# Kernel optimization log

Hardware: AMD Instinct MI355X
Metric: run time of the kernel (lower is better)

The kernel has to match this reference:

```python
import jax, jax.numpy as jnp
import numpy as np

B = 8; C = 128; EXP = 4; H = 112; W = 112; K = 3; PAD = 1; STRIDE = 1
IN_C = C * EXP  # 512
EPS = 1e-5


def setup_inputs() -> dict:
    key = jax.random.key(0)
    ks = jax.random.split(key, 24)
    f32 = jnp.float32

    def n(k, shape, s=0.05):
        return jax.random.normal(k, shape, f32) * s

    def bn_params(k):
        k1, k2, k3, k4 = jax.random.split(k, 4)
        g = 1.0 + 0.1 * jax.random.normal(k1, (), f32)  # placeholder, per-channel below
        return k1, k2, k3, k4

    inp = {}
    inp["x"] = jax.random.normal(ks[0], (B, IN_C, H, W), f32)
    # conv1: 1x1, 512 -> 128
    inp["w1"] = n(ks[1], (C, IN_C))
    inp["b1"] = n(ks[2], (C,))
    # bn1
    inp["g1"] = 1.0 + 0.1 * jax.random.normal(ks[3], (C,), f32)
    inp["be1"] = 0.1 * jax.random.normal(ks[4], (C,), f32)
    inp["m1"] = 0.1 * jax.random.normal(ks[5], (C,), f32)
    inp["v1"] = 1.0 + 0.1 * jax.random.uniform(ks[6], (C,), f32)
    # offset conv: 3x3, C -> 18 (small weights so sampling offsets stay modest)
    inp["woff"] = n(ks[7], (2 * K * K, C, K, K), 0.01)
    inp["boff"] = jnp.zeros((2 * K * K,), f32)
    # deformable conv weight: 3x3, C -> C
    inp["wd"] = n(ks[8], (C, C, K, K))
    inp["bd"] = n(ks[9], (C,))
    # bn2
    inp["g2"] = 1.0 + 0.1 * jax.random.normal(ks[10], (C,), f32)
    inp["be2"] = 0.1 * jax.random.normal(ks[11], (C,), f32)
    inp["m2"] = 0.1 * jax.random.normal(ks[12], (C,), f32)
    inp["v2"] = 1.0 + 0.1 * jax.random.uniform(ks[13], (C,), f32)
    # conv2: 1x1, 128 -> 512
    inp["w2"] = n(ks[14], (IN_C, C))
    inp["b2"] = n(ks[15], (IN_C,))
    # bn3
    inp["g3"] = 1.0 + 0.1 * jax.random.normal(ks[16], (IN_C,), f32)
    inp["be3"] = 0.1 * jax.random.normal(ks[17], (IN_C,), f32)
    inp["m3"] = 0.1 * jax.random.normal(ks[18], (IN_C,), f32)
    inp["v3"] = 1.0 + 0.1 * jax.random.uniform(ks[19], (IN_C,), f32)
    return inp


def conv1x1(x, w, b):
    return jnp.einsum("oc,bchw->bohw", w, x) + b[None, :, None, None]


def bn(x, g, be, m, v):
    inv = g / jnp.sqrt(v + EPS)
    return x * inv[None, :, None, None] + (be - m * inv)[None, :, None, None]


def conv3x3(x, w, b):
    out = jax.lax.conv_general_dilated(
        x, w, (STRIDE, STRIDE), ((PAD, PAD), (PAD, PAD)),
        dimension_numbers=("NCHW", "OIHW", "NCHW"))
    return out + b[None, :, None, None]


def deform_conv(x, offset, w, b):
    # x: [B, Cin, H, W]; offset: [B, 2*K*K, Ho, Wo] (y,x interleaved per kernel pt)
    Bn, Cin, Hh, Ww = x.shape
    Ho, Wo = offset.shape[2], offset.shape[3]
    P = Ho * Wo
    off = offset.reshape(Bn, K * K, 2, Ho, Wo)
    kk = jnp.arange(K * K)
    ky = (kk // K).astype(jnp.float32)  # 0..2
    kx = (kk % K).astype(jnp.float32)
    base_y = jnp.arange(Ho, dtype=jnp.float32) * STRIDE - PAD
    base_x = jnp.arange(Wo, dtype=jnp.float32) * STRIDE - PAD
    py = base_y[None, None, :, None] + ky[None, :, None, None] + off[:, :, 0]  # [B,9,Ho,Wo]
    px = base_x[None, None, None, :] + kx[None, :, None, None] + off[:, :, 1]
    y0 = jnp.floor(py); x0 = jnp.floor(px)
    dy = (py - y0).reshape(Bn, 1, -1)  # [B,1,9*P]
    dx = (px - x0).reshape(Bn, 1, -1)
    x_flat = x.reshape(Bn, Cin, Hh * Ww)

    def gather(yi, xi):
        valid = ((yi >= 0) & (yi <= Hh - 1) & (xi >= 0) & (xi <= Ww - 1))
        yc = jnp.clip(yi, 0, Hh - 1).astype(jnp.int32)
        xc = jnp.clip(xi, 0, Ww - 1).astype(jnp.int32)
        idx = (yc * Ww + xc).reshape(Bn, -1)  # [B, 9*P]
        g = jax.vmap(lambda xb, ib: xb[:, ib])(x_flat, idx)  # [B, Cin, 9*P]
        return g * valid.reshape(Bn, 1, -1).astype(x.dtype)

    v00 = gather(y0, x0)
    v01 = gather(y0, x0 + 1)
    v10 = gather(y0 + 1, x0)
    v11 = gather(y0 + 1, x0 + 1)
    cols = (v00 * (1 - dy) * (1 - dx) + v01 * (1 - dy) * dx
            + v10 * dy * (1 - dx) + v11 * dy * dx)  # [B, Cin, 9*P]
    cols = cols.reshape(Bn, Cin * K * K, P)
    out = jnp.einsum("oi,bip->bop", w.reshape(w.shape[0], -1), cols)
    out = out + b[None, :, None]
    return out.reshape(Bn, w.shape[0], Ho, Wo)


def reference(x, w1, b1, g1, be1, m1, v1, woff, boff, wd, bd,
              g2, be2, m2, v2, w2, b2, g3, be3, m3, v3):
    out = jax.nn.relu(bn(conv1x1(x, w1, b1), g1, be1, m1, v1))
    offset = conv3x3(out, woff, boff)
    out = deform_conv(out, offset, wd, bd)
    out = bn(out, g2, be2, m2, v2)
    out = bn(conv1x1(out, w2, b2), g3, be3, m3, v3)
    return jax.nn.relu(out + x)
```

## Files before the change

kernel.cpp:

```cpp
#include <hip/hip_runtime.h>
#include <hip/hip_bf16.h>


typedef __attribute__((ext_vector_type(8))) short short8;
typedef __attribute__((ext_vector_type(4))) float f32x4;

constexpr int Bn = 8;
constexpr int IC = 512;
constexpr int Cc = 128;
constexpr int Hh = 112;
constexpr int Ww = 112;
constexpr int Pp = Hh * Ww;
constexpr float EPSf = 1e-5f;

constexpr size_t OFS_OFFS  = 0;
constexpr size_t OFS_OUT2B = 2097152;
constexpr size_t OFS_W1B   = (size_t)Bn * Pp * IC / 2;
constexpr size_t OFS_W2B   = OFS_W1B + (size_t)Cc * IC / 2;
constexpr size_t OFS_WDB   = OFS_W2B + (size_t)IC * Cc / 2;
constexpr size_t OFS_WOFB  = OFS_WDB + (size_t)9 * Cc * Cc / 2;

__device__ __forceinline__ ushort f2bf(float f) {
  uint u = __float_as_uint(f);
  return (ushort)((u + 0x7fffu + ((u >> 16) & 1u)) >> 16);
}
__device__ __forceinline__ float bfLO(uint u) {
  return __uint_as_float(u << 16);
}
__device__ __forceinline__ float bfHI(uint u) {
  return __uint_as_float(u & 0xffff0000u);
}
__device__ __forceinline__ uint cvtpk(float a, float b) {
  __hip_bfloat162 h = __float22bfloat162_rn(make_float2(a, b));
  return *(uint*)&h;
}

__global__ __launch_bounds__(256) void prep_kernel(
    const float* __restrict__ w1, const float* __restrict__ w2,
    const float* __restrict__ wd, const float* __restrict__ woff,
    float* __restrict__ ws) {
  ushort* w1b  = (ushort*)(ws + OFS_W1B);
  ushort* w2b  = (ushort*)(ws + OFS_W2B);
  ushort* wdb  = (ushort*)(ws + OFS_WDB);
  ushort* wofb = (ushort*)(ws + OFS_WOFB);
  const int n1 = Cc * IC;
  const int n2 = IC * Cc;
  const int n3 = 9 * Cc * Cc;
  const int n4 = 9 * 32 * Cc;
  const int total = n1 + n2 + n3 + n4;
  for (int idx = blockIdx.x * blockDim.x + threadIdx.x; idx < total;
       idx += gridDim.x * blockDim.x) {
    if (idx < n1) {
      w1b[idx] = f2bf(w1[idx]);
    } else if (idx < n1 + n2) {
      int t = idx - n1;
      w2b[t] = f2bf(w2[t]);
    } else if (idx < n1 + n2 + n3) {
      int t = idx - n1 - n2;
      int k = t / (Cc * Cc), r = t % (Cc * Cc);
      int oc = r / Cc, ic = r % Cc;
      wdb[t] = f2bf(wd[(oc * Cc + ic) * 9 + k]);
    } else {
      int t = idx - n1 - n2 - n3;
      int k = t / (32 * Cc), r = t % (32 * Cc);
      int oc = r / Cc, ic = r % Cc;
      wofb[t] = (oc < 18) ? f2bf(woff[(oc * Cc + ic) * 9 + k]) : (ushort)0;
    }
  }
}

__global__ __launch_bounds__(256) void k1_fused_mfma(
    const float* __restrict__ x, const ushort* __restrict__ w1b,
    const float* __restrict__ b1, const float* __restrict__ g1,
    const float* __restrict__ be1, const float* __restrict__ m1,
    const float* __restrict__ v1, ushort* __restrict__ out1b) {
  __shared__ ushort At[64][136];

  const int tid = threadIdx.x;
  const int lane = tid & 63;
  const int wv = tid >> 6;
  const int lr = lane & 15, lg = lane >> 4;
  const int orig = blockIdx.x;
  const int bid = (orig & 7) * 196 + (orig >> 3);
  const int bi = bid / 196;
  const int p0 = (bid % 196) * 64;

  const int ic2 = (tid >> 2) * 2;
  const int pq = (tid & 3) * 4;

  const ushort* Bw = w1b + (size_t)(wv * 32) * IC;
  const float* xbase = x + (size_t)bi * IC * Pp + p0 + pq;

  f32x4 acc[4][2];
#pragma unroll
  for (int m = 0; m < 4; ++m) { acc[m][0] = (f32x4)0.f; acc[m][1] = (f32x4)0.f; }

  float4 pv0[4], pv1[4];
  {
    const float* r0 = xbase + (size_t)ic2 * Pp;
    const float* r1 = r0 + Pp;
#pragma unroll
    for (int i = 0; i < 4; ++i) {
      pv0[i] = *(const float4*)(r0 + 16 * i);
      pv1[i] = *(const float4*)(r1 + 16 * i);
    }
  }

#pragma unroll
  for (int ch = 0; ch < 4; ++ch) {
    const int c0 = ch * 128;
#pragma unroll
    for (int i = 0; i < 4; ++i) {
      int px = pq + 16 * i;
      *(uint*)&At[px + 0][ic2] = cvtpk(pv0[i].x, pv1[i].x);
      *(uint*)&At[px + 1][ic2] = cvtpk(pv0[i].y, pv1[i].y);
      *(uint*)&At[px + 2][ic2] = cvtpk(pv0[i].z, pv1[i].z);
      *(uint*)&At[px + 3][ic2] = cvtpk(pv0[i].w, pv1[i].w);
    }
    __syncthreads();

    if (ch < 3) {
      const float* r0 = xbase + (size_t)(c0 + 128 + ic2) * Pp;
      const float* r1 = r0 + Pp;
#pragma unroll
      for (int i = 0; i < 4; ++i) {
        pv0[i] = *(const float4*)(r0 + 16 * i);
        pv1[i] = *(const float4*)(r1 + 16 * i);
      }
    }

#pragma unroll
    for (int ks = 0; ks < 4; ++ks) {
      short8 b0 = *(const short8*)(Bw + (size_t)lr * IC + c0 + ks * 32 + 8 * lg);
      short8 b1v = *(const short8*)(Bw + (size_t)(16 + lr) * IC + c0 + ks * 32 + 8 * lg);
#pragma unroll
      for (int m = 0; m < 4; ++m) {
        short8 a = *(const short8*)&At[m * 16 + lr][ks * 32 + 8 * lg];
        acc[m][0] = __builtin_amdgcn_mfma_f32_16x16x32_bf16(a, b0, acc[m][0], 0, 0, 0);
        acc[m][1] = __builtin_amdgcn_mfma_f32_16x16x32_bf16(a, b1v, acc[m][1], 0, 0, 0);
      }
    }
    __syncthreads();
  }

#pragma unroll
  for (int n = 0; n < 2; ++n) {
    int oc = wv * 32 + n * 16 + lr;
    float inv = g1[oc] * rsqrtf(v1[oc] + EPSf);
    float sh = (b1[oc] - m1[oc]) * inv + be1[oc];
#pragma unroll
    for (int m = 0; m < 4; ++m) {
#pragma unroll
      for (int r = 0; r < 4; ++r) {
        int p = p0 + m * 16 + lg * 4 + r;
        out1b[((size_t)bi * Pp + p) * Cc + oc] =
            f2bf(fmaxf(acc[m][n][r] * inv + sh, 0.f));
      }
    }
  }
}

__global__ __launch_bounds__(256) void k2_offset_mfma(
    const ushort* __restrict__ out1b, const ushort* __restrict__ wofb,
    const float* __restrict__ boff, float* __restrict__ offs) {
  const int tid = threadIdx.x;
  const int lane = tid & 63;
  const int wv = tid >> 6;
  const int lr = lane & 15, lg = lane >> 4;
  const int orig = blockIdx.x;
  const int bid = (orig & 7) * 49 + (orig >> 3);
  const int bi = bid / 49;
  const int p0 = (bid % 49) * 256 + wv * 64;

  const ushort* src = out1b + (size_t)bi * Pp * Cc;

  int ohm[4], owm[4];
#pragma unroll
  for (int m = 0; m < 4; ++m) {
    int p = p0 + m * 16 + lr;
    ohm[m] = p / Ww;
    owm[m] = p - ohm[m] * Ww;
  }

  f32x4 acc[4][2];
#pragma unroll
  for (int m = 0; m < 4; ++m) { acc[m][0] = (f32x4)0.f; acc[m][1] = (f32x4)0.f; }

  for (int k = 0; k < 9; ++k) {
    const int kdy = k / 3 - 1, kdx = k % 3 - 1;
    const ushort* rp[4];
    bool val[4];
#pragma unroll
    for (int m = 0; m < 4; ++m) {
      int yy = ohm[m] + kdy, xx = owm[m] + kdx;
      val[m] = ((unsigned)yy < (unsigned)Hh) && ((unsigned)xx < (unsigned)Ww);
      int yc = min(max(yy, 0), Hh - 1), xc = min(max(xx, 0), Ww - 1);
      rp[m] = src + (size_t)(yc * Ww + xc) * Cc;
    }
#pragma unroll
    for (int ks = 0; ks < 4; ++ks) {
      short8 b0 = *(const short8*)(wofb + (size_t)(k * 32 + lr) * Cc + ks * 32 + 8 * lg);
      short8 b1v = *(const short8*)(wofb + (size_t)(k * 32 + 16 + lr) * Cc + ks * 32 + 8 * lg);
#pragma unroll
      for (int m = 0; m < 4; ++m) {
        short8 av = *(const short8*)(rp[m] + ks * 32 + 8 * lg);
        short8 a = val[m] ? av : (short8)0;
        acc[m][0] = __builtin_amdgcn_mfma_f32_16x16x32_bf16(a, b0, acc[m][0], 0, 0, 0);
        acc[m][1] = __builtin_amdgcn_mfma_f32_16x16x32_bf16(a, b1v, acc[m][1], 0, 0, 0);
      }
    }
  }

#pragma unroll
  for (int n = 0; n < 2; ++n) {
    int oc = n * 16 + lr;
    if (oc < 18) {
      float bo = boff[oc];
      float* orow = offs + ((size_t)bi * 18 + oc) * Pp;
#pragma unroll
      for (int m = 0; m < 4; ++m) {
        int p = p0 + m * 16 + lg * 4;
        float4 o;
        o.x = acc[m][n][0] + bo;
        o.y = acc[m][n][1] + bo;
        o.z = acc[m][n][2] + bo;
        o.w = acc[m][n][3] + bo;
        *(float4*)(orow + p) = o;
      }
    }
  }
}

__global__ __launch_bounds__(256) void k3_deform_mfma(
    const ushort* __restrict__ out1b, const float* __restrict__ offs,
    const ushort* __restrict__ wdb, const float* __restrict__ bd,
    const float* __restrict__ g2, const float* __restrict__ be2,
    const float* __restrict__ m2, const float* __restrict__ v2,
    ushort* __restrict__ out2b) {
  __shared__ ushort colsA[64][136];
  __shared__ float meta[9 * 64 * 8];

  const int tid = threadIdx.x;
  const int lane = tid & 63;
  const int wv = tid >> 6;
  const int lr = lane & 15, lg = lane >> 4;
  const int orig = blockIdx.x;
  const int bid = (orig & 7) * 196 + (orig >> 3);
  const int bi = bid / 196;
  const int p0 = (bid % 196) * 64;

  const ushort* src = out1b + (size_t)bi * Pp * Cc;
  const float* offb = offs + (size_t)bi * 18 * Pp;

  {
    const int p = p0 + lane;
    const int oh = p / Ww, ow = p - oh * Ww;
    for (int k = wv; k < 9; k += 4) {
      const int kdy = k / 3 - 1, kdx = k % 3 - 1;
      float py = (float)(oh + kdy) + offb[(size_t)(2 * k) * Pp + p];
      float pxf = (float)(ow + kdx) + offb[(size_t)(2 * k + 1) * Pp + p];
      float y0f = floorf(py), x0f = floorf(pxf);
      float dy = py - y0f, dx = pxf - x0f;
      int y0 = (int)y0f, x0 = (int)x0f;
      int y1 = y0 + 1, x1 = x0 + 1;
      float wy0 = (y0 >= 0 && y0 < Hh) ? 1.f - dy : 0.f;
      float wy1 = (y1 >= 0 && y1 < Hh) ? dy : 0.f;
      float wx0 = (x0 >= 0 && x0 < Ww) ? 1.f - dx : 0.f;
      float wx1 = (x1 >= 0 && x1 < Ww) ? dx : 0.f;
      int yc0 = min(max(y0, 0), Hh - 1), yc1 = min(max(y1, 0), Hh - 1);
      int xc0 = min(max(x0, 0), Ww - 1), xc1 = min(max(x1, 0), Ww - 1);
      float* mp = &meta[(k * 64 + lane) * 8];
      mp[0] = wy0 * wx0;
      mp[1] = wy0 * wx1;
      mp[2] = wy1 * wx0;
      mp[3] = wy1 * wx1;
      int* ip = (int*)(mp + 4);
      ip[0] = (yc0 * Ww + xc0) * (Cc * 2);
      ip[1] = (yc0 * Ww + xc1) * (Cc * 2);
      ip[2] = (yc1 * Ww + xc0) * (Cc * 2);
      ip[3] = (yc1 * Ww + xc1) * (Cc * 2);
    }
  }
  __syncthreads();

  f32x4 acc[4][2];
#pragma unroll
  for (int m = 0; m < 4; ++m) { acc[m][0] = (f32x4)0.f; acc[m][1] = (f32x4)0.f; }

  const int half = lane >> 5;
  const int l32 = lane & 31;
  const char* sb = (const char*)src + l32 * 8;

  for (int k = 0; k < 9; ++k) {
#pragma unroll 4
    for (int t = 0; t < 8; ++t) {
      const int px = wv * 16 + 2 * t + half;
      const float* mp = &meta[(k * 64 + px) * 8];
      float4 w4 = *(const float4*)mp;
      int4 o4 = *(const int4*)(mp + 4);
      uint2 v00 = *(const uint2*)(sb + o4.x);
      uint2 v01 = *(const uint2*)(sb + o4.y);
      uint2 v10 = *(const uint2*)(sb + o4.z);
      uint2 v11 = *(const uint2*)(sb + o4.w);
      float c0 = w4.x * bfLO(v00.x) + w4.y * bfLO(v01.x)
               + w4.z * bfLO(v10.x) + w4.w * bfLO(v11.x);
      float c1 = w4.x * bfHI(v00.x) + w4.y * bfHI(v01.x)
               + w4.z * bfHI(v10.x) + w4.w * bfHI(v11.x);
      float c2 = w4.x * bfLO(v00.y) + w4.y * bfLO(v01.y)
               + w4.z * bfLO(v10.y) + w4.w * bfLO(v11.y);
      float c3 = w4.x * bfHI(v00.y) + w4.y * bfHI(v01.y)
               + w4.z * bfHI(v10.y) + w4.w * bfHI(v11.y);
      uint2 packed;
      packed.x = cvtpk(c0, c1);
      packed.y = cvtpk(c2, c3);
      *(uint2*)&colsA[px][l32 * 4] = packed;
    }
    __syncthreads();

    const ushort* wk = wdb + (size_t)k * Cc * Cc + (size_t)(wv * 32) * Cc;
#pragma unroll
    for (int ks = 0; ks < 4; ++ks) {
      short8 b0 = *(const short8*)(wk + lr * Cc + ks * 32 + 8 * lg);
      short8 b1v = *(const short8*)(wk + (16 + lr) * Cc + ks * 32 + 8 * lg);
#pragma unroll
      for (int m = 0; m < 4; ++m) {
        short8 a = *(const short8*)&colsA[m * 16 + lr][ks * 32 + 8 * lg];
        acc[m][0] = __builtin_amdgcn_mfma_f32_16x16x32_bf16(a, b0, acc[m][0], 0, 0, 0);
        acc[m][1] = __builtin_amdgcn_mfma_f32_16x16x32_bf16(a, b1v, acc[m][1], 0, 0, 0);
      }
    }
    __syncthreads();
  }

#pragma unroll
  for (int n = 0; n < 2; ++n) {
    int oc = wv * 32 + n * 16 + lr;
    float inv = g2[oc] * rsqrtf(v2[oc] + EPSf);
    float sh = (bd[oc] - m2[oc]) * inv + be2[oc];
#pragma unroll
    for (int m = 0; m < 4; ++m) {
#pragma unroll
      for (int r = 0; r < 4; ++r) {
        int p = p0 + m * 16 + lg * 4 + r;
        out2b[((size_t)bi * Pp + p) * Cc + oc] = f2bf(acc[m][n][r] * inv + sh);
      }
    }
  }
}

__global__ __launch_bounds__(256, 2) void k4_mfma(
    const ushort* __restrict__ out2b, const ushort* __restrict__ w2b,
    const float* __restrict__ b2, const float* __restrict__ g3,
    const float* __restrict__ be3, const float* __restrict__ m3,
    const float* __restrict__ v3, const float* __restrict__ x,
    float* __restrict__ out) {
  const int tid = threadIdx.x;
  const int lane = tid & 63;
  const int wv = tid >> 6;
  const int lr = lane & 15, lg = lane >> 4;
  const int orig = blockIdx.x;
  const int bid = (orig & 7) * 392 + (orig >> 3);
  const int bi = bid / 392;
  const int r392 = bid % 392;
  const int oc_t = r392 / 49;
  const int p0 = (r392 % 49) * 256 + wv * 64;
  const int ocb = oc_t * 64;

  const ushort* A = out2b + ((size_t)bi * Pp + p0) * Cc;
  const ushort* Bw = w2b + (size_t)ocb * Cc;

  float4 xv[4][4];
#pragma unroll
  for (int n = 0; n < 4; ++n) {
    int oc = ocb + n * 16 + lr;
    const float* xr = x + ((size_t)bi * IC + oc) * Pp + p0 + lg * 4;
#pragma unroll
    for (int m = 0; m < 4; ++m) xv[n][m] = *(const float4*)(xr + m * 16);
  }

  f32x4 acc[4][4];
#pragma unroll
  for (int m = 0; m < 4; ++m)
#pragma unroll
    for (int n = 0; n < 4; ++n) acc[m][n] = (f32x4)0.f;

#pragma unroll
  for (int ks = 0; ks < 4; ++ks) {
    short8 a[4];
#pragma unroll
    for (int m = 0; m < 4; ++m)
      a[m] = *(const short8*)(A + (size_t)(m * 16 + lr) * Cc + ks * 32 + 8 * lg);
#pragma unroll
    for (int n = 0; n < 4; ++n) {
      short8 b = *(const short8*)(Bw + (size_t)(n * 16 + lr) * Cc + ks * 32 + 8 * lg);
#pragma unroll
      for (int m = 0; m < 4; ++m)
        acc[m][n] = __builtin_amdgcn_mfma_f32_16x16x32_bf16(a[m], b, acc[m][n], 0, 0, 0);
    }
  }

#pragma unroll
  for (int n = 0; n < 4; ++n) {
    int oc = ocb + n * 16 + lr;
    float inv = g3[oc] * rsqrtf(v3[oc] + EPSf);
    float sh = (b2[oc] - m3[oc]) * inv + be3[oc];
    float* orow = out + ((size_t)bi * IC + oc) * Pp + p0 + lg * 4;
#pragma unroll
    for (int m = 0; m < 4; ++m) {
      float4 o;
      o.x = fmaxf(acc[m][n][0] * inv + sh + xv[n][m].x, 0.f);
      o.y = fmaxf(acc[m][n][1] * inv + sh + xv[n][m].y, 0.f);
      o.z = fmaxf(acc[m][n][2] * inv + sh + xv[n][m].z, 0.f);
      o.w = fmaxf(acc[m][n][3] * inv + sh + xv[n][m].w, 0.f);
      *(float4*)(orow + m * 16) = o;
    }
  }
}

extern "C" void kernel_launch(void* const* d_in, const int* in_sizes, int n_in,
                              void* d_out, int out_size, void* d_ws, size_t ws_size,
                              hipStream_t stream) {
  const float* x    = (const float*)d_in[0];
  const float* w1   = (const float*)d_in[1];
  const float* b1   = (const float*)d_in[2];
  const float* g1   = (const float*)d_in[3];
  const float* be1  = (const float*)d_in[4];
  const float* m1   = (const float*)d_in[5];
  const float* v1   = (const float*)d_in[6];
  const float* woff = (const float*)d_in[7];
  const float* boff = (const float*)d_in[8];
  const float* wd   = (const float*)d_in[9];
  const float* bd   = (const float*)d_in[10];
  const float* g2   = (const float*)d_in[11];
  const float* be2  = (const float*)d_in[12];
  const float* m2   = (const float*)d_in[13];
  const float* v2   = (const float*)d_in[14];
  const float* w2   = (const float*)d_in[15];
  const float* b2   = (const float*)d_in[16];
  const float* g3   = (const float*)d_in[17];
  const float* be3  = (const float*)d_in[18];
  const float* m3   = (const float*)d_in[19];
  const float* v3   = (const float*)d_in[20];

  float* ws   = (float*)d_ws;
  float* out  = (float*)d_out;
  float*  offs  = ws + OFS_OFFS;
  ushort* out2b = (ushort*)(ws + OFS_OUT2B);
  ushort* w1b   = (ushort*)(ws + OFS_W1B);
  ushort* w2b   = (ushort*)(ws + OFS_W2B);
  ushort* wdb   = (ushort*)(ws + OFS_WDB);
  ushort* wofb  = (ushort*)(ws + OFS_WOFB);
  ushort* out1b = (ushort*)d_out;

  prep_kernel<<<512, 256, 0, stream>>>(w1, w2, wd, woff, ws);
  k1_fused_mfma<<<Bn * 196, 256, 0, stream>>>(x, w1b, b1, g1, be1, m1, v1, out1b);
  k2_offset_mfma<<<Bn * 49, 256, 0, stream>>>(out1b, wofb, boff, offs);
  k3_deform_mfma<<<Bn * 196, 256, 0, stream>>>(out1b, offs, wdb, bd,
                                               g2, be2, m2, v2, out2b);
  k4_mfma<<<Bn * 392, 256, 0, stream>>>(out2b, w2b, b2, g3, be3, m3, v3, x, out);
}
```

Before: 373.6 us.

## Double-buffer deformable column tile and overlap bilinear gathers with MFMA

The deform kernel now keeps two column buffers in LDS. Gathers for the next kernel tap are issued before the current tap's MFMA work and committed in halves between its k-steps, so gather latency is hidden behind matrix math. Each lane also gathers 16-byte vectors covering 8 channels, where it used to take 8 bytes, so a quarter-wave handles one pixel. This adds LDS usage and holds many more gathered values in registers, which could lower occupancy. It also removes one barrier per tap.

```diff
diff --git a/kernel.cpp b/kernel.cpp
--- a/kernel.cpp
+++ b/kernel.cpp
@@ -237,7 +237,7 @@
     const float* __restrict__ g2, const float* __restrict__ be2,
     const float* __restrict__ m2, const float* __restrict__ v2,
     ushort* __restrict__ out2b) {
-  __shared__ ushort colsA[64][136];
+  __shared__ ushort colsA[2][64][136];
   __shared__ float meta[9 * 64 * 8];
 
   const int tid = threadIdx.x;
@@ -287,50 +287,89 @@
 #pragma unroll
   for (int m = 0; m < 4; ++m) { acc[m][0] = (f32x4)0.f; acc[m][1] = (f32x4)0.f; }
 
-  const int half = lane >> 5;
-  const int l32 = lane & 31;
-  const char* sb = (const char*)src + l32 * 8;
+  const int pxq = lane >> 4;
+  const int l16 = lane & 15;
+  const char* sb = (const char*)src + l16 * 16;
+
+  uint4 gv[4][4];
+  float4 gw[4];
+
+#define ISSUE(kk, t)                                                     \
+  {                                                                      \
+    const int px_ = wv * 16 + (t) * 4 + pxq;                             \
+    const float* mp_ = &meta[((kk) * 64 + px_) * 8];                     \
+    gw[t] = *(const float4*)mp_;                                         \
+    int4 o4_ = *(const int4*)(mp_ + 4);                                  \
+    gv[t][0] = *(const uint4*)(sb + o4_.x);                              \
+    gv[t][1] = *(const uint4*)(sb + o4_.y);                              \
+    gv[t][2] = *(const uint4*)(sb + o4_.z);                              \
+    gv[t][3] = *(const uint4*)(sb + o4_.w);                              \
+  }
+
+#define COMMIT(buf, t)                                                   \
+  {                                                                      \
+    const int px_ = wv * 16 + (t) * 4 + pxq;                             \
+    float4 w4_ = gw[t];                                                  \
+    uint4 pk_;                                                           \
+    uint* pkp_ = (uint*)&pk_;                                            \
+    _Pragma("unroll")                                                    \
+    for (int j = 0; j < 4; ++j) {                                        \
+      uint a0_ = ((const uint*)&gv[t][0])[j];                            \
+      uint a1_ = ((const uint*)&gv[t][1])[j];                            \
+      uint a2_ = ((const uint*)&gv[t][2])[j];                            \
+      uint a3_ = ((const uint*)&gv[t][3])[j];                            \
+      float lo_ = w4_.x * bfLO(a0_) + w4_.y * bfLO(a1_)                  \
+                + w4_.z * bfLO(a2_) + w4_.w * bfLO(a3_);                 \
+      float hi_ = w4_.x * bfHI(a0_) + w4_.y * bfHI(a1_)                  \
+                + w4_.z * bfHI(a2_) + w4_.w * bfHI(a3_);                 \
+      pkp_[j] = cvtpk(lo_, hi_);                                         \
+    }                                                                    \
+    *(uint4*)&colsA[buf][px_][l16 * 8] = pk_;                            \
+  }
+
+  ISSUE(0, 0) ISSUE(0, 1) ISSUE(0, 2) ISSUE(0, 3)
+  COMMIT(0, 0) COMMIT(0, 1) COMMIT(0, 2) COMMIT(0, 3)
+  __syncthreads();
 
   for (int k = 0; k < 9; ++k) {
-#pragma unroll 4
-    for (int t = 0; t < 8; ++t) {
-      const int px = wv * 16 + 2 * t + half;
-      const float* mp = &meta[(k * 64 + px) * 8];
-      float4 w4 = *(const float4*)mp;
-      int4 o4 = *(const int4*)(mp + 4);
-      uint2 v00 = *(const uint2*)(sb + o4.x);
-      uint2 v01 = *(const uint2*)(sb + o4.y);
-      uint2 v10 = *(const uint2*)(sb + o4.z);
-      uint2 v11 = *(const uint2*)(sb + o4.w);
-      float c0 = w4.x * bfLO(v00.x) + w4.y * bfLO(v01.x)
-               + w4.z * bfLO(v10.x) + w4.w * bfLO(v11.x);
-      float c1 = w4.x * bfHI(v00.x) + w4.y * bfHI(v01.x)
-               + w4.z * bfHI(v10.x) + w4.w * bfHI(v11.x);
-      float c2 = w4.x * bfLO(v00.y) + w4.y * bfLO(v01.y)
-               + w4.z * bfLO(v10.y) + w4.w * bfLO(v11.y);
-      float c3 = w4.x * bfHI(v00.y) + w4.y * bfHI(v01.y)
-               + w4.z * bfHI(v10.y) + w4.w * bfHI(v11.y);
-      uint2 packed;
-      packed.x = cvtpk(c0, c1);
-      packed.y = cvtpk(c2, c3);
-      *(uint2*)&colsA[px][l32 * 4] = packed;
-    }
-    __syncthreads();
-
+    const int cur = k & 1;
+    const int nxt = cur ^ 1;
     const ushort* wk = wdb + (size_t)k * Cc * Cc + (size_t)(wv * 32) * Cc;
-#pragma unroll
-    for (int ks = 0; ks < 4; ++ks) {
+
+    if (k < 8) { ISSUE(k + 1, 0) ISSUE(k + 1, 1) }
+
+#pragma unroll
+    for (int ks = 0; ks < 2; ++ks) {
       short8 b0 = *(const short8*)(wk + lr * Cc + ks * 32 + 8 * lg);
       short8 b1v = *(const short8*)(wk + (16 + lr) * Cc + ks * 32 + 8 * lg);
 #pragma unroll
       for (int m = 0; m < 4; ++m) {
-        short8 a = *(const short8*)&colsA[m * 16 + lr][ks * 32 + 8 * lg];
+        short8 a = *(const short8*)&colsA[cur][m * 16 + lr][ks * 32 + 8 * lg];
         acc[m][0] = __builtin_amdgcn_mfma_f32_16x16x32_bf16(a, b0, acc[m][0], 0, 0, 0);
         acc[m][1] = __builtin_amdgcn_mfma_f32_16x16x32_bf16(a, b1v, acc[m][1], 0, 0, 0);
       }
     }
+
+    if (k < 8) { COMMIT(nxt, 0) COMMIT(nxt, 1) ISSUE(k + 1, 2) ISSUE(k + 1, 3) }
+
+#pragma unroll
+    for (int ks = 2; ks < 4; ++ks) {
+      short8 b0 = *(const short8*)(wk + lr * Cc + ks * 32 + 8 * lg);
+      short8 b1v = *(const short8*)(wk + (16 + lr) * Cc + ks * 32 + 8 * lg);
+#pragma unroll
+      for (int m = 0; m < 4; ++m) {
+        short8 a = *(const short8*)&colsA[cur][m * 16 + lr][ks * 32 + 8 * lg];
+        acc[m][0] = __builtin_amdgcn_mfma_f32_16x16x32_bf16(a, b0, acc[m][0], 0, 0, 0);
+        acc[m][1] = __builtin_amdgcn_mfma_f32_16x16x32_bf16(a, b1v, acc[m][1], 0, 0, 0);
+      }
+    }
+
+    if (k < 8) { COMMIT(nxt, 2) COMMIT(nxt, 3) }
     __syncthreads();
   }
+
+#undef ISSUE
+#undef COMMIT
 
 #pragma unroll
   for (int n = 0; n < 2; ++n) {
```

Result: faster. 355.4 us (-4.9%).
